# Optimization experiments

Measured on AMD Instinct MI355X. Metric: run time of the kernel, lower is better.

Reference implementation:

```python
import jax, jax.numpy as jnp
import numpy as np

NUM_HEADS = 6


def setup_inputs() -> dict:
    key = jax.random.key(0)
    k1, k2, k3 = jax.random.split(key, 3)
    b_, n, c = 512, 256, 192
    nw = 64
    x = jax.random.normal(k1, (b_, n, c), dtype=jnp.float32)
    mask = jnp.zeros((nw, n, n), dtype=jnp.float32)  # 0 / -inf additive window mask
    W_qkv = jax.random.normal(k2, (3 * c, c), dtype=jnp.float32) * 0.02
    W_proj = jax.random.normal(k3, (c, c), dtype=jnp.float32) * 0.02
    b_proj = jnp.zeros((c,), dtype=jnp.float32)
    return {"x": x, "mask": mask, "W_qkv": W_qkv, "W_proj": W_proj, "b_proj": b_proj}


def reference(x, mask, W_qkv, W_proj, b_proj):
    b_, n, c = x.shape
    h = NUM_HEADS
    d = c // h
    scale = d ** (-0.5)
    # qkv projection (no bias): (b_, n, 3, h, d) -> (3, b_, h, n, d)
    qkv = (x @ W_qkv.T).reshape(b_, n, 3, h, d).transpose(2, 0, 3, 1, 4)
    q, k, v = qkv[0], qkv[1], qkv[2]
    q = q * scale
    attn = jnp.einsum('bhid,bhjd->bhij', q, k)  # (b_, h, n, n)
    nw = mask.shape[0]
    # add per-window mask bias: view as (B, nw, h, n, n) + (1, nw, 1, n, n)
    attn = attn.reshape(b_ // nw, nw, h, n, n) + mask[None, :, None, :, :]
    attn = attn.reshape(b_, h, n, n)
    attn = jax.nn.softmax(attn, axis=-1)
    out = jnp.einsum('bhij,bhjd->bhid', attn, v)  # (b_, h, n, d)
    out = out.transpose(0, 2, 1, 3).reshape(b_, n, c)
    return out @ W_proj.T + b_proj
```

## Files before the change

### kernel.cpp

```cpp
#include <hip/hip_runtime.h>
#include <hip/hip_bf16.h>
#include <stdint.h>

typedef short bf16x8 __attribute__((ext_vector_type(8)));
typedef float f32x4 __attribute__((ext_vector_type(4)));

#define B_   512
#define N_   256
#define C_   192
#define H_   6
#define D_   32
#define NW_  64

__device__ __forceinline__ uint16_t f2bf(float f) {
    uint32_t u = __builtin_bit_cast(uint32_t, f);
    u += 0x7FFFu + ((u >> 16) & 1u);
    return (uint16_t)(u >> 16);
}

__device__ __forceinline__ uint32_t pk_bf16(float a, float b) {
    float2 t; t.x = a; t.y = b;
    __hip_bfloat162 h = __float22bfloat162_rn(t);
    uint32_t u;
    __builtin_memcpy(&u, &h, 4);
    return u;
}

__device__ __forceinline__ bf16x8 ld_bf8(const uint16_t* p) {
    uint4 u = *reinterpret_cast<const uint4*>(p);
    return __builtin_bit_cast(bf16x8, u);
}

__global__ __launch_bounds__(256)
void prep_kernel(const float* __restrict__ mask,
                 const float* __restrict__ wqkv,
                 const float* __restrict__ wproj,
                 uint16_t* __restrict__ sel,
                 uint16_t* __restrict__ wqkv_bf,
                 uint16_t* __restrict__ wproj_bf,
                 unsigned* __restrict__ flag) {
    const int CS = 524288;
    const int CQ = 13824;
    const int CP = 4608;
    int i = blockIdx.x * blockDim.x + threadIdx.x;
    int stride = gridDim.x * blockDim.x;
    bool nz = false;
    for (int c = i; c < CS + CQ + CP; c += stride) {
        if (c < CS) {
            const float4* mp = reinterpret_cast<const float4*>(mask) + (int64_t)c * 2;
            float4 a = mp[0], b = mp[1];
            nz |= (a.x != 0.f) | (a.y != 0.f) | (a.z != 0.f) | (a.w != 0.f) |
                  (b.x != 0.f) | (b.y != 0.f) | (b.z != 0.f) | (b.w != 0.f);
            uint4 o;
            o.x = (a.x == 0.f ? 0xFFFFu : 0u) | ((a.y == 0.f ? 0xFFFFu : 0u) << 16);
            o.y = (a.z == 0.f ? 0xFFFFu : 0u) | ((a.w == 0.f ? 0xFFFFu : 0u) << 16);
            o.z = (b.x == 0.f ? 0xFFFFu : 0u) | ((b.y == 0.f ? 0xFFFFu : 0u) << 16);
            o.w = (b.z == 0.f ? 0xFFFFu : 0u) | ((b.w == 0.f ? 0xFFFFu : 0u) << 16);
            *reinterpret_cast<uint4*>(sel + (int64_t)c * 8) = o;
        } else if (c < CS + CQ) {
            int j = c - CS;
            const float4* wp4 = reinterpret_cast<const float4*>(wqkv) + (int64_t)j * 2;
            float4 a = wp4[0], b = wp4[1];
            uint4 o;
            o.x = pk_bf16(a.x, a.y); o.y = pk_bf16(a.z, a.w);
            o.z = pk_bf16(b.x, b.y); o.w = pk_bf16(b.z, b.w);
            *reinterpret_cast<uint4*>(wqkv_bf + (int64_t)j * 8) = o;
        } else {
            int j = c - CS - CQ;
            const float4* wp4 = reinterpret_cast<const float4*>(wproj) + (int64_t)j * 2;
            float4 a = wp4[0], b = wp4[1];
            uint4 o;
            o.x = pk_bf16(a.x, a.y); o.y = pk_bf16(a.z, a.w);
            o.z = pk_bf16(b.x, b.y); o.w = pk_bf16(b.z, b.w);
            *reinterpret_cast<uint4*>(wproj_bf + (int64_t)j * 8) = o;
        }
    }
    if (flag && __any(nz) && ((threadIdx.x & 63) == 0))
        atomicOr(flag, 1u);
}

#define SA 200
#define SB 72
__global__ __launch_bounds__(512, 4)
void qkv_kernel(const float* __restrict__ x, const uint16_t* __restrict__ wq,
                uint16_t* __restrict__ qbuf, uint16_t* __restrict__ kbuf,
                uint16_t* __restrict__ vtbuf) {
    __shared__ __align__(16) uint16_t Alds[128 * SA];
    __shared__ __align__(16) uint16_t Blds[192 * SB];
    const int tid  = threadIdx.x;
    const int lane = tid & 63;
    const int wv   = tid >> 6;
    const int wrow = wv >> 2;
    const int wcol = wv & 3;
    const int quad = lane >> 4;
    const int l15  = lane & 15;
    const int m0   = blockIdx.x * 128;

#pragma unroll
    for (int p = 0; p < 12; p++) {
        int f = p * 512 + tid;
        int row = f / 48, c4 = f % 48;
        const float4 v = *reinterpret_cast<const float4*>(
            x + (int64_t)(m0 + row) * 192 + c4 * 4);
        uint2 d;
        d.x = pk_bf16(v.x, v.y);
        d.y = pk_bf16(v.z, v.w);
        *reinterpret_cast<uint2*>(&Alds[row * SA + c4 * 4]) = d;
    }

    const float scale = 0.17677669529663687f * 1.4426950408889634f;

    for (int cb = 0; cb < 3; cb++) {
        f32x4 acc[4][3];
#pragma unroll
        for (int i = 0; i < 4; i++)
#pragma unroll
            for (int j = 0; j < 3; j++) acc[i][j] = (f32x4)0.f;

        for (int k0 = 0; k0 < 192; k0 += 64) {
            __syncthreads();
#pragma unroll
            for (int p = 0; p < 3; p++) {
                int u = p * 512 + tid;
                int row = u >> 3, c8 = u & 7;
                uint4 w = *reinterpret_cast<const uint4*>(
                    wq + (int64_t)(cb * 192 + row) * 192 + k0 + c8 * 8);
                *reinterpret_cast<uint4*>(&Blds[row * SB + c8 * 8]) = w;
            }
            __syncthreads();
#pragma unroll
            for (int ks = 0; ks < 2; ks++) {
                bf16x8 xf[4], wf[3];
#pragma unroll
                for (int i = 0; i < 4; i++)
                    xf[i] = *reinterpret_cast<const bf16x8*>(
                        &Alds[(wrow * 64 + i * 16 + l15) * SA + k0 + ks * 32 + quad * 8]);
#pragma unroll
                for (int j = 0; j < 3; j++)
                    wf[j] = *reinterpret_cast<const bf16x8*>(
                        &Blds[(wcol * 48 + j * 16 + l15) * SB + ks * 32 + quad * 8]);
                if (cb < 2) {
#pragma unroll
                    for (int i = 0; i < 4; i++)
#pragma unroll
                        for (int j = 0; j < 3; j++)
                            acc[i][j] = __builtin_amdgcn_mfma_f32_16x16x32_bf16(
                                wf[j], xf[i], acc[i][j], 0, 0, 0);
                } else {
#pragma unroll
                    for (int i = 0; i < 4; i++)
#pragma unroll
                        for (int j = 0; j < 3; j++)
                            acc[i][j] = __builtin_amdgcn_mfma_f32_16x16x32_bf16(
                                xf[i], wf[j], acc[i][j], 0, 0, 0);
                }
            }
        }

        if (cb < 2) {
            uint16_t* dst = (cb == 0) ? qbuf : kbuf;
            const float sc = (cb == 0) ? scale : 1.0f;
#pragma unroll
            for (int i = 0; i < 4; i++) {
                int m = m0 + wrow * 64 + i * 16 + l15;
                int b = m >> 8, pos = m & 255;
#pragma unroll
                for (int j = 0; j < 3; j++) {
                    int cbase = wcol * 48 + j * 16 + quad * 4;
                    int h = cbase >> 5, d0 = cbase & 31;
                    int64_t bh = (int64_t)b * H_ + h;
                    uint2 s;
                    s.x = pk_bf16(acc[i][j][0] * sc, acc[i][j][1] * sc);
                    s.y = pk_bf16(acc[i][j][2] * sc, acc[i][j][3] * sc);
                    *reinterpret_cast<uint2*>(&dst[(bh * N_ + pos) * D_ + d0]) = s;
                }
            }
        } else {
#pragma unroll
            for (int i = 0; i < 4; i++) {
                int m = m0 + wrow * 64 + i * 16 + quad * 4;
                int b = m >> 8, pos0 = m & 255;
#pragma unroll
                for (int j = 0; j < 3; j++) {
                    int c = wcol * 48 + j * 16 + l15;
                    int h = c >> 5, d = c & 31;
                    int64_t bh = (int64_t)b * H_ + h;
                    uint2 s;
                    s.x = pk_bf16(acc[i][j][0], acc[i][j][1]);
                    s.y = pk_bf16(acc[i][j][2], acc[i][j][3]);
                    *reinterpret_cast<uint2*>(&vtbuf[(bh * D_ + d) * N_ + pos0]) = s;
                }
            }
        }
    }
}

__global__ __launch_bounds__(256, 3)
void attn_kernel(const uint16_t* __restrict__ qbuf, const uint16_t* __restrict__ kbuf,
                 const uint16_t* __restrict__ vtbuf, const uint16_t* __restrict__ sel,
                 const unsigned* __restrict__ flag,
                 uint16_t* __restrict__ aout) {
    __shared__ __align__(16) uint16_t Plds[4 * 2 * 32 * 40];
    const int bi = blockIdx.x;
    const int h  = bi % 6;
    const int r_ = bi / 6;
    const int ih = r_ & 1;
    const int g  = (r_ >> 1) & 7;
    const int w  = r_ >> 4;
    const int b  = g * 64 + w;
    const int tid  = threadIdx.x;
    const int lane = tid & 63;
    const int wv   = tid >> 6;
    const int quad = lane >> 4;
    const int l15  = lane & 15;
    const int i0   = ih * 128 + wv * 32;
    const bool hasmask = flag ? (*flag != 0u) : true;
    const int64_t bh = (int64_t)b * H_ + h;
    const uint16_t* qB = qbuf  + bh * N_ * D_;
    const uint16_t* kB = kbuf  + bh * N_ * D_;
    const uint16_t* vB = vtbuf + bh * D_ * N_;
    const uint16_t* sB = sel   + (int64_t)w * N_ * N_;
    uint16_t* Pw = &Plds[wv * 2 * 32 * 40];

    bf16x8 qf[2];
#pragma unroll
    for (int it = 0; it < 2; it++)
        qf[it] = ld_bf8(&qB[(i0 + it * 16 + l15) * D_ + quad * 8]);

    f32x4 oacc[2][2];
    f32x4 lacc[2];
#pragma unroll
    for (int mt = 0; mt < 2; mt++) {
        oacc[mt][0] = (f32x4)0.f; oacc[mt][1] = (f32x4)0.f; lacc[mt] = (f32x4)0.f;
    }
    bf16x8 ones;
#pragma unroll
    for (int e = 0; e < 8; e++) ones[e] = (short)0x3F80;

    bf16x8 kf[4];
#pragma unroll
    for (int jt = 0; jt < 4; jt++)
        kf[jt] = ld_bf8(&kB[(jt * 16 + l15) * D_ + quad * 8]);
    bf16x8 vf[2][2];
#pragma unroll
    for (int hf = 0; hf < 2; hf++)
#pragma unroll
        for (int nt = 0; nt < 2; nt++)
            vf[hf][nt] = ld_bf8(&vB[(nt * 16 + l15) * N_ + hf * 32 + quad * 8]);

    for (int jc = 0; jc < 4; jc++) {
        const int j0 = jc * 64;

        bf16x8 kfn[4], vfn[2][2];
        if (jc < 3) {
#pragma unroll
            for (int jt = 0; jt < 4; jt++)
                kfn[jt] = ld_bf8(&kB[(j0 + 64 + jt * 16 + l15) * D_ + quad * 8]);
#pragma unroll
            for (int hf = 0; hf < 2; hf++)
#pragma unroll
                for (int nt = 0; nt < 2; nt++)
                    vfn[hf][nt] = ld_bf8(&vB[(nt * 16 + l15) * N_ + j0 + 64 + hf * 32 + quad * 8]);
        }

        uint4 sv[2][2];
        if (hasmask) {
#pragma unroll
            for (int hf = 0; hf < 2; hf++)
#pragma unroll
                for (int mt = 0; mt < 2; mt++)
                    sv[hf][mt] = *reinterpret_cast<const uint4*>(
                        &sB[(int64_t)(i0 + mt * 16 + l15) * N_ + j0 + hf * 32 + quad * 8]);
        } else {
#pragma unroll
            for (int hf = 0; hf < 2; hf++)
#pragma unroll
                for (int mt = 0; mt < 2; mt++)
                    sv[hf][mt] = make_uint4(~0u, ~0u, ~0u, ~0u);
        }

#pragma unroll
        for (int hf = 0; hf < 2; hf++) {
            f32x4 sacc[2][2];
#pragma unroll
            for (int jt2 = 0; jt2 < 2; jt2++)
#pragma unroll
                for (int it = 0; it < 2; it++) sacc[jt2][it] = (f32x4)0.f;
            __builtin_amdgcn_s_setprio(1);
#pragma unroll
            for (int jt2 = 0; jt2 < 2; jt2++)
#pragma unroll
                for (int it = 0; it < 2; it++)
                    sacc[jt2][it] = __builtin_amdgcn_mfma_f32_16x16x32_bf16(
                        kf[hf * 2 + jt2], qf[it], sacc[jt2][it], 0, 0, 0);
            __builtin_amdgcn_s_setprio(0);

            uint16_t* Ph = Pw + hf * (32 * 40);
#pragma unroll
            for (int it = 0; it < 2; it++)
#pragma unroll
                for (int jt2 = 0; jt2 < 2; jt2++) {
                    f32x4 s = sacc[jt2][it];
                    uint2 d;
                    d.x = pk_bf16(__builtin_amdgcn_exp2f(s[0]),
                                  __builtin_amdgcn_exp2f(s[1]));
                    d.y = pk_bf16(__builtin_amdgcn_exp2f(s[2]),
                                  __builtin_amdgcn_exp2f(s[3]));
                    *reinterpret_cast<uint2*>(
                        &Ph[(it * 16 + l15) * 40 + jt2 * 16 + quad * 4]) = d;
                }

#pragma unroll
            for (int mt = 0; mt < 2; mt++) {
                uint4 p = *reinterpret_cast<const uint4*>(
                    &Ph[(mt * 16 + l15) * 40 + quad * 8]);
                p.x &= sv[hf][mt].x; p.y &= sv[hf][mt].y;
                p.z &= sv[hf][mt].z; p.w &= sv[hf][mt].w;
                bf16x8 pa = __builtin_bit_cast(bf16x8, p);
                __builtin_amdgcn_s_setprio(1);
                oacc[mt][0] = __builtin_amdgcn_mfma_f32_16x16x32_bf16(pa, vf[hf][0], oacc[mt][0], 0, 0, 0);
                oacc[mt][1] = __builtin_amdgcn_mfma_f32_16x16x32_bf16(pa, vf[hf][1], oacc[mt][1], 0, 0, 0);
                lacc[mt]    = __builtin_amdgcn_mfma_f32_16x16x32_bf16(pa, ones,      lacc[mt],    0, 0, 0);
                __builtin_amdgcn_s_setprio(0);
            }
        }

        if (jc < 3) {
#pragma unroll
            for (int jt = 0; jt < 4; jt++) kf[jt] = kfn[jt];
#pragma unroll
            for (int hf = 0; hf < 2; hf++)
#pragma unroll
                for (int nt = 0; nt < 2; nt++) vf[hf][nt] = vfn[hf][nt];
        }
    }

#pragma unroll
    for (int mt = 0; mt < 2; mt++)
#pragma unroll
        for (int r4 = 0; r4 < 4; r4++) {
            float inv = 1.0f / lacc[mt][r4];
            int i = i0 + mt * 16 + quad * 4 + r4;
#pragma unroll
            for (int nt = 0; nt < 2; nt++) {
                float v = oacc[mt][nt][r4] * inv;
                aout[((int64_t)b * N_ + i) * C_ + h * 32 + nt * 16 + l15] = f2bf(v);
            }
        }
}

__global__ __launch_bounds__(512, 4)
void proj_kernel(const uint16_t* __restrict__ a, const uint16_t* __restrict__ wp,
                 const float* __restrict__ bias, float* __restrict__ out) {
    __shared__ __align__(16) uint16_t Alds[128 * SA];
    const int tid  = threadIdx.x;
    const int lane = tid & 63;
    const int wv   = tid >> 6;
    const int wm   = wv >> 2;
    const int wn   = wv & 3;
    const int quad = lane >> 4;
    const int l15  = lane & 15;
    const int m0   = blockIdx.x * 128;

#pragma unroll
    for (int p = 0; p < 6; p++) {
        int u = p * 512 + tid;
        int row = u / 24, c8 = u % 24;
        uint4 v = *reinterpret_cast<const uint4*>(
            a + (int64_t)(m0 + row) * 192 + c8 * 8);
        *reinterpret_cast<uint4*>(&Alds[row * SA + c8 * 8]) = v;
    }
    __syncthreads();

    f32x4 acc[4][3];
#pragma unroll
    for (int x = 0; x < 4; x++)
#pragma unroll
        for (int y = 0; y < 3; y++) acc[x][y] = (f32x4)0.f;

    const uint16_t* wB = wp + (int64_t)(wn * 48 + l15) * 192;
    bf16x8 bfr[3], bfn[3];
#pragma unroll
    for (int nt = 0; nt < 3; nt++)
        bfr[nt] = ld_bf8(wB + nt * 16 * 192 + quad * 8);

#pragma unroll
    for (int kk = 0; kk < 6; kk++) {
        const int kb = kk * 32;
        if (kk < 5) {
#pragma unroll
            for (int nt = 0; nt < 3; nt++)
                bfn[nt] = ld_bf8(wB + nt * 16 * 192 + kb + 32 + quad * 8);
        }
        bf16x8 af[4];
#pragma unroll
        for (int mt = 0; mt < 4; mt++)
            af[mt] = *reinterpret_cast<const bf16x8*>(
                &Alds[(wm * 64 + mt * 16 + l15) * SA + kb + quad * 8]);
#pragma unroll
        for (int mt = 0; mt < 4; mt++)
#pragma unroll
            for (int nt = 0; nt < 3; nt++)
                acc[mt][nt] = __builtin_amdgcn_mfma_f32_16x16x32_bf16(
                    af[mt], bfr[nt], acc[mt][nt], 0, 0, 0);
        if (kk < 5) {
#pragma unroll
            for (int nt = 0; nt < 3; nt++) bfr[nt] = bfn[nt];
        }
    }

    float bv[3];
#pragma unroll
    for (int nt = 0; nt < 3; nt++) bv[nt] = bias[wn * 48 + nt * 16 + l15];
#pragma unroll
    for (int mt = 0; mt < 4; mt++)
#pragma unroll
        for (int r = 0; r < 4; r++) {
            int m = m0 + wm * 64 + mt * 16 + quad * 4 + r;
#pragma unroll
            for (int nt = 0; nt < 3; nt++) {
                int col = wn * 48 + nt * 16 + l15;
                out[(int64_t)m * 192 + col] = acc[mt][nt][r] + bv[nt];
            }
        }
}

extern "C" void kernel_launch(void* const* d_in, const int* in_sizes, int n_in,
                              void* d_out, int out_size, void* d_ws, size_t ws_size,
                              hipStream_t stream) {
    const float* x     = (const float*)d_in[0];
    const float* mask  = (const float*)d_in[1];
    const float* wqkv  = (const float*)d_in[2];
    const float* wproj = (const float*)d_in[3];
    const float* bproj = (const float*)d_in[4];
    float* out = (float*)d_out;

    uint16_t* qbuf = (uint16_t*)d_out;
    uint16_t* kbuf = qbuf + 25165824;
    char* ws = (char*)d_ws;
    uint16_t* vtbuf = (uint16_t*)(ws);
    uint16_t* aout  = (uint16_t*)(ws + 50331648);
    uint16_t* sel   = (uint16_t*)(ws + 100663296);
    uint16_t* wq_bf = (uint16_t*)(ws + 109051904);
    uint16_t* wp_bf = (uint16_t*)(ws + 109273088);
    unsigned* flag  = nullptr;
    if (ws_size >= 109346816 + 4)
        flag = (unsigned*)(ws + 109346816);

    if (flag) hipMemsetAsync(flag, 0, 4, stream);
    prep_kernel<<<2048, 256, 0, stream>>>(mask, wqkv, wproj, sel, wq_bf, wp_bf, flag);
    qkv_kernel<<<1024, 512, 0, stream>>>(x, wq_bf, qbuf, kbuf, vtbuf);
    attn_kernel<<<6144, 256, 0, stream>>>(qbuf, kbuf, vtbuf, sel, flag, aout);
    proj_kernel<<<1024, 512, 0, stream>>>(aout, wp_bf, bproj, out);
}
```

Measured before the change: 330.4 us.

## Load QKV weight fragments directly into registers and shrink qkv tile to 64 rows

```diff
diff --git a/kernel.cpp b/kernel.cpp
--- a/kernel.cpp
+++ b/kernel.cpp
@@ -80,25 +80,21 @@
 }
 
 #define SA 200
-#define SB 72
-__global__ __launch_bounds__(512, 4)
+__global__ __launch_bounds__(256, 3)
 void qkv_kernel(const float* __restrict__ x, const uint16_t* __restrict__ wq,
                 uint16_t* __restrict__ qbuf, uint16_t* __restrict__ kbuf,
                 uint16_t* __restrict__ vtbuf) {
-    __shared__ __align__(16) uint16_t Alds[128 * SA];
-    __shared__ __align__(16) uint16_t Blds[192 * SB];
+    __shared__ __align__(16) uint16_t Alds[64 * SA];
     const int tid  = threadIdx.x;
     const int lane = tid & 63;
     const int wv   = tid >> 6;
-    const int wrow = wv >> 2;
-    const int wcol = wv & 3;
     const int quad = lane >> 4;
     const int l15  = lane & 15;
-    const int m0   = blockIdx.x * 128;
+    const int m0   = blockIdx.x * 64;
 
 #pragma unroll
     for (int p = 0; p < 12; p++) {
-        int f = p * 512 + tid;
+        int f = p * 256 + tid;
         int row = f / 48, c4 = f % 48;
         const float4 v = *reinterpret_cast<const float4*>(
             x + (int64_t)(m0 + row) * 192 + c4 * 4);
@@ -107,66 +103,61 @@
         d.y = pk_bf16(v.z, v.w);
         *reinterpret_cast<uint2*>(&Alds[row * SA + c4 * 4]) = d;
     }
+    __syncthreads();
 
     const float scale = 0.17677669529663687f * 1.4426950408889634f;
 
     for (int cb = 0; cb < 3; cb++) {
+        const uint16_t* wB = wq + ((int64_t)cb * 192 + wv * 48 + l15) * 192;
+        bf16x8 wf[3][6];
+#pragma unroll
+        for (int j = 0; j < 3; j++)
+#pragma unroll
+            for (int kk = 0; kk < 6; kk++)
+                wf[j][kk] = ld_bf8(wB + j * 16 * 192 + kk * 32 + quad * 8);
+
         f32x4 acc[4][3];
 #pragma unroll
         for (int i = 0; i < 4; i++)
 #pragma unroll
             for (int j = 0; j < 3; j++) acc[i][j] = (f32x4)0.f;
 
-        for (int k0 = 0; k0 < 192; k0 += 64) {
-            __syncthreads();
-#pragma unroll
-            for (int p = 0; p < 3; p++) {
-                int u = p * 512 + tid;
-                int row = u >> 3, c8 = u & 7;
-                uint4 w = *reinterpret_cast<const uint4*>(
-                    wq + (int64_t)(cb * 192 + row) * 192 + k0 + c8 * 8);
-                *reinterpret_cast<uint4*>(&Blds[row * SB + c8 * 8]) = w;
-            }
-            __syncthreads();
-#pragma unroll
-            for (int ks = 0; ks < 2; ks++) {
-                bf16x8 xf[4], wf[3];
+#pragma unroll
+        for (int kk = 0; kk < 6; kk++) {
+            bf16x8 xf[4];
+#pragma unroll
+            for (int i = 0; i < 4; i++)
+                xf[i] = *reinterpret_cast<const bf16x8*>(
+                    &Alds[(i * 16 + l15) * SA + kk * 32 + quad * 8]);
+            if (cb < 2) {
 #pragma unroll
                 for (int i = 0; i < 4; i++)
-                    xf[i] = *reinterpret_cast<const bf16x8*>(
-                        &Alds[(wrow * 64 + i * 16 + l15) * SA + k0 + ks * 32 + quad * 8]);
-#pragma unroll
-                for (int j = 0; j < 3; j++)
-                    wf[j] = *reinterpret_cast<const bf16x8*>(
-                        &Blds[(wcol * 48 + j * 16 + l15) * SB + ks * 32 + quad * 8]);
-                if (cb < 2) {
-#pragma unroll
-                    for (int i = 0; i < 4; i++)
-#pragma unroll
-                        for (int j = 0; j < 3; j++)
-                            acc[i][j] = __builtin_amdgcn_mfma_f32_16x16x32_bf16(
-                                wf[j], xf[i], acc[i][j], 0, 0, 0);
-                } else {
-#pragma unroll
-                    for (int i = 0; i < 4; i++)
-#pragma unroll
-                        for (int j = 0; j < 3; j++)
-                            acc[i][j] = __builtin_amdgcn_mfma_f32_16x16x32_bf16(
-                                xf[i], wf[j], acc[i][j], 0, 0, 0);
-                }
-            }
-        }
+#pragma unroll
+                    for (int j = 0; j < 3; j++)
+                        acc[i][j] = __builtin_amdgcn_mfma_f32_16x16x32_bf16(
+                            wf[j][kk], xf[i], acc[i][j], 0, 0, 0);
+            } else {
+#pragma unroll
+                for (int i = 0; i < 4; i++)
+#pragma unroll
+                    for (int j = 0; j < 3; j++)
+                        acc[i][j] = __builtin_amdgcn_mfma_f32_16x16x32_bf16(
+                            xf[i], wf[j][kk], acc[i][j], 0, 0, 0);
+            }
+        }
+
+        __syncthreads();
 
         if (cb < 2) {
             uint16_t* dst = (cb == 0) ? qbuf : kbuf;
             const float sc = (cb == 0) ? scale : 1.0f;
 #pragma unroll
             for (int i = 0; i < 4; i++) {
-                int m = m0 + wrow * 64 + i * 16 + l15;
+                int m = m0 + i * 16 + l15;
                 int b = m >> 8, pos = m & 255;
 #pragma unroll
                 for (int j = 0; j < 3; j++) {
-                    int cbase = wcol * 48 + j * 16 + quad * 4;
+                    int cbase = wv * 48 + j * 16 + quad * 4;
                     int h = cbase >> 5, d0 = cbase & 31;
                     int64_t bh = (int64_t)b * H_ + h;
                     uint2 s;
@@ -178,11 +169,11 @@
         } else {
 #pragma unroll
             for (int i = 0; i < 4; i++) {
-                int m = m0 + wrow * 64 + i * 16 + quad * 4;
+                int m = m0 + i * 16 + quad * 4;
                 int b = m >> 8, pos0 = m & 255;
 #pragma unroll
                 for (int j = 0; j < 3; j++) {
-                    int c = wcol * 48 + j * 16 + l15;
+                    int c = wv * 48 + j * 16 + l15;
                     int h = c >> 5, d = c & 31;
                     int64_t bh = (int64_t)b * H_ + h;
                     uint2 s;
@@ -449,7 +440,7 @@
 
     if (flag) hipMemsetAsync(flag, 0, 4, stream);
     prep_kernel<<<2048, 256, 0, stream>>>(mask, wqkv, wproj, sel, wq_bf, wp_bf, flag);
-    qkv_kernel<<<1024, 512, 0, stream>>>(x, wq_bf, qbuf, kbuf, vtbuf);
+    qkv_kernel<<<2048, 256, 0, stream>>>(x, wq_bf, qbuf, kbuf, vtbuf);
     attn_kernel<<<6144, 256, 0, stream>>>(qbuf, kbuf, vtbuf, sel, flag, aout);
     proj_kernel<<<1024, 512, 0, stream>>>(aout, wp_bf, bproj, out);
 }
```

Measured after the change: 353.9 us. 7.1% more time.
